# Optimization experiments

Measured on AMD Instinct MI355X. Metric: run time of the kernel, lower is better.

## Reference

```python
import jax, jax.numpy as jnp
import numpy as np

DIM = 256
HEADS = 8
K_RATIO = 0.25


def setup_inputs() -> dict:
    key = jax.random.key(0)
    ks = jax.random.split(key, 5)
    B, C, S = 4, DIM, 2048
    x = jax.random.normal(ks[0], (B, C, S), dtype=jnp.float32)
    # Conv1d(dim, 3*dim, 1, bias=False) weight -> (3*dim, dim)
    W_qkv = jax.random.normal(ks[1], (3 * DIM, DIM), dtype=jnp.float32) * (1.0 / np.sqrt(DIM))
    # depthwise Conv1d(3*dim, 3*dim, 3, groups=3*dim) weight -> (3*dim, 1, 3)
    W_dw = jax.random.normal(ks[2], (3 * DIM, 1, 3), dtype=jnp.float32) * (1.0 / np.sqrt(3))
    # Conv1d(dim, dim, 1, bias=False) weight -> (dim, dim)
    W_proj = jax.random.normal(ks[3], (DIM, DIM), dtype=jnp.float32) * (1.0 / np.sqrt(DIM))
    temperature = jnp.ones((HEADS, 1, 1), dtype=jnp.float32)
    return {"x": x, "W_qkv": W_qkv, "W_dw": W_dw, "W_proj": W_proj,
            "temperature": temperature}


def _l2norm(t, eps=1e-12):
    # F.normalize: x / max(||x||_2, eps)
    n = jnp.sqrt(jnp.sum(t * t, axis=-1, keepdims=True))
    return t / jnp.maximum(n, eps)


def reference(x, W_qkv, W_dw, W_proj, temperature):
    B, C, S = x.shape
    H = temperature.shape[0]
    hd = C // H
    # 1x1 conv == channel matmul
    qkv = jnp.einsum('oc,bcs->bos', W_qkv, x)  # [B, 3C, S]
    # depthwise conv, kernel 3, pad 1
    qkv = jax.lax.conv_general_dilated(
        qkv, W_dw, window_strides=(1,), padding=[(1, 1)],
        dimension_numbers=('NCH', 'OIH', 'NCH'),
        feature_group_count=3 * C)
    q, k, v = jnp.split(qkv, 3, axis=1)  # each [B, C, S]

    def to_heads(t):
        return t.reshape(B, H, hd, S).transpose(0, 1, 3, 2)  # [B, H, S, hd]

    q = _l2norm(to_heads(q))
    k = _l2norm(to_heads(k))
    v = to_heads(v)

    scores = jnp.einsum('bhsc,bhtc->bhst', q, k) * temperature  # [B,H,S,S]

    topk = max(1, min(S, int(np.ceil(K_RATIO * S))))
    vals, idx = jax.lax.top_k(scores, topk)  # [B,H,S,topk]

    # scatter top-k values into a -inf tensor along the last axis
    N = B * H * S
    sparse = jnp.full((N, S), -jnp.inf, dtype=scores.dtype)
    rows = jnp.arange(N)[:, None]
    sparse = sparse.at[rows, idx.reshape(N, topk)].set(vals.reshape(N, topk))
    sparse = jnp.clip(sparse.reshape(B, H, S, S), -10000.0, 10000.0)

    attn = jax.nn.softmax(sparse, axis=-1)  # dropout p=0.0 -> identity
    out = jnp.einsum('bhst,bhtc->bhsc', attn, v)  # [B,H,S,hd]
    out = out.transpose(0, 1, 3, 2).reshape(B, C, S)  # b (head c) s
    return jnp.einsum('oc,bcs->bos', W_proj, out)
```

## Files before the change

### kernel.cpp

```cpp
#include <hip/hip_runtime.h>
#include <math.h>

typedef __attribute__((ext_vector_type(8))) short short8;
typedef __attribute__((ext_vector_type(4))) float f32x4;
typedef __attribute__((ext_vector_type(2))) float f32x2;
typedef __attribute__((ext_vector_type(2))) unsigned int uint2v;
typedef __attribute__((ext_vector_type(4))) unsigned int uint4v;

#define DEV __device__ __forceinline__

static constexpr int B_ = 4, C_ = 256, S_ = 2048, H_ = 8, O3_ = 768;
static constexpr int TOPK = 512;
static constexpr int QT = 16;
static constexpr int QCOLS = 512;
static constexpr int QSTR = 516;
static constexpr int QBUF = 16 * QSTR;
static constexpr int PSTH = 1024;
static constexpr int P1OFF = 2 * QBUF;
static constexpr size_t K3_LDS_BYTES = (size_t)2 * QBUF * 4;
static constexpr int XSTR = 40;

DEV unsigned cvt_pk_bf16(float a, float b) {
  unsigned r;
  asm("v_cvt_pk_bf16_f32 %0, %1, %2" : "=v"(r) : "v"(a), "v"(b));
  return r;
}
DEV unsigned short f2bf1(float f) { return (unsigned short)(cvt_pk_bf16(f, f) & 0xFFFFu); }
DEV float bf2f(unsigned short h) { return __uint_as_float(((unsigned)h) << 16); }
DEV void hilo(float f, unsigned short& h, unsigned short& l) {
  unsigned p = cvt_pk_bf16(f, f);
  h = (unsigned short)p;
  float r = f - __uint_as_float(p << 16);
  l = (unsigned short)(cvt_pk_bf16(r, r) & 0xFFFFu);
}

__global__ void k_convw(const float* __restrict__ wqkv, const float* __restrict__ wproj,
                        unsigned short* __restrict__ wq_hi, unsigned short* __restrict__ wq_lo,
                        unsigned short* __restrict__ wproj_bf) {
  int i = blockIdx.x * 256 + threadIdx.x;
  if (i < O3_ * C_) {
    unsigned short h, l;
    hilo(wqkv[i], h, l);
    wq_hi[i] = h;
    wq_lo[i] = l;
  }
  if (i < C_ * C_) wproj_bf[i] = f2bf1(wproj[i]);
}

__global__ __launch_bounds__(256) void k_qkv(const unsigned short* __restrict__ w_hi,
                                             const unsigned short* __restrict__ w_lo,
                                             const float* __restrict__ x,
                                             float* __restrict__ raw) {
  __shared__ unsigned short xh[2][64 * XSTR];
  __shared__ unsigned short xl[2][64 * XSTR];
  int b = blockIdx.z;
  int m0 = blockIdx.y * 64, n0 = blockIdx.x * 64;
  int tid = threadIdx.x, lane = tid & 63, wid = tid >> 6;
  int l15 = lane & 15, lh = lane >> 4;
  int wm = (wid >> 1) * 32, wn = (wid & 1) * 32;
  int sl = tid & 63, cg = tid >> 6;
  const float* xb = x + (size_t)b * C_ * S_ + n0 + sl;

  f32x4 acc[2][2] = {};
  int mA = m0 + wm + l15;

  auto stage = [&](int k0, int bufi) {
    float f[8];
#pragma unroll
    for (int j = 0; j < 8; ++j)
      f[j] = xb[(size_t)(k0 + cg * 8 + j) * S_];
    unsigned h[4], l[4];
#pragma unroll
    for (int j = 0; j < 4; ++j) {
      h[j] = cvt_pk_bf16(f[2 * j], f[2 * j + 1]);
      float r0 = f[2 * j] - __uint_as_float(h[j] << 16);
      float r1 = f[2 * j + 1] - __uint_as_float(h[j] & 0xFFFF0000u);
      l[j] = cvt_pk_bf16(r0, r1);
    }
    int o = sl * XSTR + cg * 8;
    *(uint4v*)&xh[bufi][o] = uint4v{h[0], h[1], h[2], h[3]};
    *(uint4v*)&xl[bufi][o] = uint4v{l[0], l[1], l[2], l[3]};
  };

  stage(0, 0);
  for (int ks = 0; ks < 8; ++ks) {
    __syncthreads();
    if (ks < 7) stage((ks + 1) * 32, (ks ^ 1) & 1);
    int kk = lh * 8;
    int k0 = ks * 32;
    const unsigned short* bh0 = &xh[ks & 1][(wn + l15) * XSTR + kk];
    const unsigned short* bh1 = &xh[ks & 1][(wn + 16 + l15) * XSTR + kk];
    const unsigned short* bl0 = &xl[ks & 1][(wn + l15) * XSTR + kk];
    const unsigned short* bl1 = &xl[ks & 1][(wn + 16 + l15) * XSTR + kk];
    short8 b0h = *(const short8*)bh0;
    short8 b1h = *(const short8*)bh1;
    short8 b0l = *(const short8*)bl0;
    short8 b1l = *(const short8*)bl1;
    short8 a0h = *(const short8*)(w_hi + (size_t)mA * C_ + k0 + kk);
    short8 a1h = *(const short8*)(w_hi + (size_t)(mA + 16) * C_ + k0 + kk);
    short8 a0l = *(const short8*)(w_lo + (size_t)mA * C_ + k0 + kk);
    short8 a1l = *(const short8*)(w_lo + (size_t)(mA + 16) * C_ + k0 + kk);
    acc[0][0] = __builtin_amdgcn_mfma_f32_16x16x32_bf16(a0h, b0h, acc[0][0], 0, 0, 0);
    acc[0][1] = __builtin_amdgcn_mfma_f32_16x16x32_bf16(a0h, b1h, acc[0][1], 0, 0, 0);
    acc[1][0] = __builtin_amdgcn_mfma_f32_16x16x32_bf16(a1h, b0h, acc[1][0], 0, 0, 0);
    acc[1][1] = __builtin_amdgcn_mfma_f32_16x16x32_bf16(a1h, b1h, acc[1][1], 0, 0, 0);
    acc[0][0] = __builtin_amdgcn_mfma_f32_16x16x32_bf16(a0h, b0l, acc[0][0], 0, 0, 0);
    acc[0][1] = __builtin_amdgcn_mfma_f32_16x16x32_bf16(a0h, b1l, acc[0][1], 0, 0, 0);
    acc[1][0] = __builtin_amdgcn_mfma_f32_16x16x32_bf16(a1h, b0l, acc[1][0], 0, 0, 0);
    acc[1][1] = __builtin_amdgcn_mfma_f32_16x16x32_bf16(a1h, b1l, acc[1][1], 0, 0, 0);
    acc[0][0] = __builtin_amdgcn_mfma_f32_16x16x32_bf16(a0l, b0h, acc[0][0], 0, 0, 0);
    acc[0][1] = __builtin_amdgcn_mfma_f32_16x16x32_bf16(a0l, b1h, acc[0][1], 0, 0, 0);
    acc[1][0] = __builtin_amdgcn_mfma_f32_16x16x32_bf16(a1l, b0h, acc[1][0], 0, 0, 0);
    acc[1][1] = __builtin_amdgcn_mfma_f32_16x16x32_bf16(a1l, b1h, acc[1][1], 0, 0, 0);
  }
  float* rawb = raw + (size_t)b * O3_ * S_;
#pragma unroll
  for (int i = 0; i < 2; ++i)
#pragma unroll
    for (int j = 0; j < 2; ++j)
#pragma unroll
      for (int r = 0; r < 4; ++r) {
        int row = m0 + wm + i * 16 + lh * 4 + r;
        int col = n0 + wn + j * 16 + l15;
        rawb[(size_t)row * S_ + col] = acc[i][j][r];
      }
}

DEV float conv3(const float* __restrict__ rp, const float* __restrict__ w, int s) {
  float a = (s > 0) ? rp[s - 1] : 0.f;
  float b = rp[s];
  float c = (s < S_ - 1) ? rp[s + 1] : 0.f;
  return w[0] * a + w[1] * b + w[2] * c;
}

__global__ __launch_bounds__(256) void k_dwnorm(const float* __restrict__ raw,
                                                const float* __restrict__ wdw,
                                                const float* __restrict__ temp,
                                                unsigned short* __restrict__ q_hi,
                                                unsigned short* __restrict__ q_lo,
                                                unsigned short* __restrict__ k_hi,
                                                unsigned short* __restrict__ k_lo,
                                                unsigned short* __restrict__ vt) {
  int b = blockIdx.z, h = blockIdx.y;
  int tid = threadIdx.x;
  int wave = tid >> 6, lane = tid & 63;
  int dg = lane & 7;
  int sl = lane >> 3;
  int s = blockIdx.x * 32 + wave * 8 + sl;
  const float* rawb = raw + (size_t)b * O3_ * S_;
  float tph = temp[h];
  size_t bh = (size_t)(b * H_ + h);
  float qv[4], kv[4], vv[4];
  float sq = 0.f, sk = 0.f;
#pragma unroll
  for (int dd = 0; dd < 4; ++dd) {
    int d = dg * 4 + dd;
    int oq = h * 32 + d;
    float q = conv3(rawb + (size_t)oq * S_, wdw + oq * 3, s);
    qv[dd] = q; sq += q * q;
    int ok = oq + 256;
    float k = conv3(rawb + (size_t)ok * S_, wdw + ok * 3, s);
    kv[dd] = k; sk += k * k;
    int ov = oq + 512;
    vv[dd] = conv3(rawb + (size_t)ov * S_, wdw + ov * 3, s);
  }
#pragma unroll
  for (int m = 1; m < 8; m <<= 1) {
    sq += __shfl_xor(sq, m);
    sk += __shfl_xor(sk, m);
  }
  float iq = tph / fmaxf(sqrtf(sq), 1e-12f);
  float ik = 1.f / fmaxf(sqrtf(sk), 1e-12f);
  size_t base = (bh * S_ + s) * 32 + dg * 4;

  float q0 = qv[0] * iq, q1 = qv[1] * iq, q2 = qv[2] * iq, q3 = qv[3] * iq;
  unsigned qh01 = cvt_pk_bf16(q0, q1), qh23 = cvt_pk_bf16(q2, q3);
  *(uint2v*)(q_hi + base) = uint2v{qh01, qh23};
  float ql0 = q0 - __uint_as_float(qh01 << 16);
  float ql1 = q1 - __uint_as_float(qh01 & 0xFFFF0000u);
  float ql2 = q2 - __uint_as_float(qh23 << 16);
  float ql3 = q3 - __uint_as_float(qh23 & 0xFFFF0000u);
  *(uint2v*)(q_lo + base) = uint2v{cvt_pk_bf16(ql0, ql1), cvt_pk_bf16(ql2, ql3)};

  float k0 = kv[0] * ik, k1 = kv[1] * ik, k2 = kv[2] * ik, k3 = kv[3] * ik;
  unsigned kh01 = cvt_pk_bf16(k0, k1), kh23 = cvt_pk_bf16(k2, k3);
  *(uint2v*)(k_hi + base) = uint2v{kh01, kh23};
  float kl0 = k0 - __uint_as_float(kh01 << 16);
  float kl1 = k1 - __uint_as_float(kh01 & 0xFFFF0000u);
  float kl2 = k2 - __uint_as_float(kh23 << 16);
  float kl3 = k3 - __uint_as_float(kh23 & 0xFFFF0000u);
  *(uint2v*)(k_lo + base) = uint2v{cvt_pk_bf16(kl0, kl1), cvt_pk_bf16(kl2, kl3)};

#pragma unroll
  for (int dd = 0; dd < 4; ++dd) {
    int d = dg * 4 + dd;
    vt[(bh * 32 + d) * S_ + s] = f2bf1(vv[dd]);
  }
}

__global__ __launch_bounds__(1024, 8) void k_attn(const unsigned short* __restrict__ q_hi,
                                                  const unsigned short* __restrict__ q_lo,
                                                  const unsigned short* __restrict__ k_hi,
                                                  const unsigned short* __restrict__ k_lo,
                                                  const unsigned short* __restrict__ vt,
                                                  unsigned short* __restrict__ ao) {
  extern __shared__ float smem[];
  __shared__ float is_arr[QT];
  unsigned short* Pb = (unsigned short*)smem;
  float* red = smem;
  int bid = blockIdx.x;
  int tile = bid & 127;
  int bh = bid >> 7;
  int q0 = tile * QT;
  int tid = threadIdx.x, lane = tid & 63, wv = tid >> 6;
  int l15 = lane & 15, lh = lane >> 4;
  const unsigned short* vb = vt + (size_t)bh * 32 * S_;

  size_t qoff = ((size_t)bh * S_ + q0 + l15) * 32 + lh * 8;
  short8 ah = *(const short8*)(q_hi + qoff);
  short8 al = *(const short8*)(q_lo + qoff);
  size_t kbase = (size_t)bh * S_ * 32;

  float v[32];

  short8 kh0, kl0, kh1, kl1;
  {
    const unsigned short* kp = k_hi + kbase + (size_t)(wv * 32 + l15) * 32 + lh * 8;
    const unsigned short* lp = k_lo + kbase + (size_t)(wv * 32 + l15) * 32 + lh * 8;
    kh0 = *(const short8*)(kp);       kl0 = *(const short8*)(lp);
    kh1 = *(const short8*)(kp + 512); kl1 = *(const short8*)(lp + 512);
  }
#pragma unroll
  for (int qq = 0; qq < 4; ++qq) {
    float* buf = smem + (qq & 1) * QBUF;
    {
      f32x4 d0 = {}, d1 = {};
      __builtin_amdgcn_s_setprio(1);
      d0 = __builtin_amdgcn_mfma_f32_16x16x32_bf16(ah, kh0, d0, 0, 0, 0);
      d0 = __builtin_amdgcn_mfma_f32_16x16x32_bf16(ah, kl0, d0, 0, 0, 0);
      d0 = __builtin_amdgcn_mfma_f32_16x16x32_bf16(al, kh0, d0, 0, 0, 0);
      d1 = __builtin_amdgcn_mfma_f32_16x16x32_bf16(ah, kh1, d1, 0, 0, 0);
      d1 = __builtin_amdgcn_mfma_f32_16x16x32_bf16(ah, kl1, d1, 0, 0, 0);
      d1 = __builtin_amdgcn_mfma_f32_16x16x32_bf16(al, kh1, d1, 0, 0, 0);
      __builtin_amdgcn_s_setprio(0);
      int tloc = wv * 32 + l15;
#pragma unroll
      for (int r = 0; r < 4; ++r) {
        buf[(lh * 4 + r) * QSTR + tloc] = d0[r];
        buf[(lh * 4 + r) * QSTR + tloc + 16] = d1[r];
      }
      if (qq < 3) {
        int colg = (qq + 1) * QCOLS + wv * 32;
        const unsigned short* kp = k_hi + kbase + (size_t)(colg + l15) * 32 + lh * 8;
        const unsigned short* lp = k_lo + kbase + (size_t)(colg + l15) * 32 + lh * 8;
        kh0 = *(const short8*)(kp);       kl0 = *(const short8*)(lp);
        kh1 = *(const short8*)(kp + 512); kl1 = *(const short8*)(lp + 512);
      }
    }
    __syncthreads();
#pragma unroll
    for (int kk2 = 0; kk2 < 4; ++kk2) {
      f32x2 pr = *(const f32x2*)&buf[wv * QSTR + kk2 * 128 + 2 * lane];
      v[qq * 8 + kk2 * 2] = pr[0];
      v[qq * 8 + kk2 * 2 + 1] = pr[1];
    }
  }

  {
    float vmax = v[0], vmin = v[0], sum = 0.f, sqs = 0.f;
#pragma unroll
    for (int j = 0; j < 32; ++j) {
      vmax = fmaxf(vmax, v[j]); vmin = fminf(vmin, v[j]);
      sum += v[j]; sqs = fmaf(v[j], v[j], sqs);
    }
#pragma unroll
    for (int m = 1; m < 64; m <<= 1) {
      vmax = fmaxf(vmax, __shfl_xor(vmax, m));
      vmin = fminf(vmin, __shfl_xor(vmin, m));
      sum += __shfl_xor(sum, m);
      sqs += __shfl_xor(sqs, m);
    }
    float mu = sum * (1.f / 2048.f);
    float sig = sqrtf(fmaxf(sqs * (1.f / 2048.f) - mu * mu, 0.f));

    float vlo = vmin - 1e-3f, vhi = vmax;
    float flo = 1536.f, fhi = -512.f;
    int chi = 0;
    float T = vhi;
    bool exact = false;
    int lastside = 0;
    float piv = mu + 0.67449f * sig;
    if (!(piv > vlo && piv < vhi)) piv = 0.5f * (vlo + vhi);
    for (int it = 0; it < 32; ++it) {
      int c = 0;
#pragma unroll
      for (int j = 0; j < 32; ++j)
        c += (int)__popcll(__ballot(v[j] > piv));
      if (c == TOPK) { T = piv; exact = true; break; }
      if (c > TOPK) {
        if (lastside == 1) fhi *= 0.5f;
        vlo = piv; flo = (float)(c - TOPK); lastside = 1;
      } else {
        if (lastside == -1) flo *= 0.5f;
        vhi = piv; fhi = (float)(c - TOPK); chi = c; lastside = -1;
      }
      float npiv;
      if (it == 0 && sig > 1e-20f) {
        float z = (piv - mu) / sig;
        float dens = 0.398942f * __expf(-0.5f * z * z) * (2048.f / sig);
        npiv = piv + (float)(c - TOPK) / fmaxf(dens, 1e-6f);
      } else {
        npiv = vhi - fhi * (vhi - vlo) / (fhi - flo);
      }
      if (!(npiv > vlo && npiv < vhi)) npiv = 0.5f * (vlo + vhi);
      if (!(npiv > vlo && npiv < vhi)) break;
      piv = npiv;
    }
    int cntGT = exact ? TOPK : chi;
    if (!exact) T = vhi;

    unsigned selbits = 0;
#pragma unroll
    for (int j = 0; j < 32; ++j)
      if (v[j] > T) selbits |= (1u << j);
    int need = TOPK - cntGT;
    if (need > 0) {
      int base = 0;
      unsigned long long lmask = (lane == 0) ? 0ull : (~0ull >> (64 - lane));
#pragma unroll
      for (int k = 0; k < 16; ++k) {
        bool t0 = (v[2 * k] == T), t1 = (v[2 * k + 1] == T);
        unsigned long long m0 = __ballot(t0);
        unsigned long long m1 = __ballot(t1);
        int before = base + (int)__popcll(m0 & lmask) + (int)__popcll(m1 & lmask);
        int r0 = before;
        int r1 = before + (t0 ? 1 : 0);
        if (t0 && r0 < need) selbits |= (1u << (2 * k));
        if (t1 && r1 < need) selbits |= (1u << (2 * k + 1));
        base += (int)__popcll(m0) + (int)__popcll(m1);
      }
    }

    float ssum = 0.f;
#pragma unroll
    for (int j = 0; j < 32; ++j) {
      float e = ((selbits >> j) & 1u) ? __expf(v[j] - vmax) : 0.f;
      v[j] = e;
      ssum += e;
    }
#pragma unroll
    for (int m = 1; m < 64; m <<= 1) ssum += __shfl_xor(ssum, m);
    if (lane == 0) is_arr[wv] = 1.f / ssum;
  }

  f32x4 acc0 = {}, acc1 = {};
  int swz_w = (wv & 7) << 3;
  int swz_r = (l15 & 7) << 3;
#pragma unroll
  for (int kk = 0; kk < 8; ++kk) {
    int lc = (kk >> 2) * 512 + (kk & 3) * 128 + 2 * lane;
    unsigned pk = cvt_pk_bf16(v[2 * kk], v[2 * kk + 1]);
    *(unsigned*)&Pb[(wv * PSTH + lc) ^ swz_w] = pk;
  }
  __syncthreads();
  {
#pragma unroll
    for (int kk = 0; kk < 8; ++kk) {
      int lc = (kk >> 2) * 512 + (kk & 3) * 128 + 2 * lane;
      unsigned pk = cvt_pk_bf16(v[16 + 2 * kk], v[16 + 2 * kk + 1]);
      *(unsigned*)&Pb[P1OFF + ((wv * PSTH + lc) ^ swz_w)] = pk;
    }
    const unsigned short* v0p = vb + (size_t)l15 * S_ + wv * 64 + lh * 8;
    const unsigned short* v1p = v0p + 16 * S_;
#pragma unroll
    for (int kt = 0; kt < 2; ++kt) {
      int lc = wv * 64 + kt * 32 + lh * 8;
      short8 a = *(const short8*)(Pb + ((l15 * PSTH + lc) ^ swz_r));
      short8 b0 = *(const short8*)(v0p + kt * 32);
      short8 b1 = *(const short8*)(v1p + kt * 32);
      __builtin_amdgcn_s_setprio(1);
      acc0 = __builtin_amdgcn_mfma_f32_16x16x32_bf16(a, b0, acc0, 0, 0, 0);
      acc1 = __builtin_amdgcn_mfma_f32_16x16x32_bf16(a, b1, acc1, 0, 0, 0);
      __builtin_amdgcn_s_setprio(0);
    }
  }
  __syncthreads();
  {
    const unsigned short* v0p = vb + (size_t)l15 * S_ + 1024 + wv * 64 + lh * 8;
    const unsigned short* v1p = v0p + 16 * S_;
#pragma unroll
    for (int kt = 0; kt < 2; ++kt) {
      int lc = wv * 64 + kt * 32 + lh * 8;
      short8 a = *(const short8*)(Pb + P1OFF + ((l15 * PSTH + lc) ^ swz_r));
      short8 b0 = *(const short8*)(v0p + kt * 32);
      short8 b1 = *(const short8*)(v1p + kt * 32);
      __builtin_amdgcn_s_setprio(1);
      acc0 = __builtin_amdgcn_mfma_f32_16x16x32_bf16(a, b0, acc0, 0, 0, 0);
      acc1 = __builtin_amdgcn_mfma_f32_16x16x32_bf16(a, b1, acc1, 0, 0, 0);
      __builtin_amdgcn_s_setprio(0);
    }
  }
  __syncthreads();

#pragma unroll
  for (int r = 0; r < 4; ++r) {
    red[wv * 529 + (lh * 4 + r) * 33 + l15] = acc0[r];
    red[wv * 529 + (lh * 4 + r) * 33 + 16 + l15] = acc1[r];
  }
  __syncthreads();
  if (tid < 512) {
    int row = tid >> 5, d = tid & 31;
    float s = 0.f;
#pragma unroll
    for (int w = 0; w < 16; ++w) s += red[w * 529 + row * 33 + d];
    s *= is_arr[row];
    ao[((size_t)bh * S_ + q0 + row) * 32 + d] = f2bf1(s);
  }
}

__global__ __launch_bounds__(256) void k_proj(const unsigned short* __restrict__ wbf,
                                              const unsigned short* __restrict__ ao,
                                              float* __restrict__ out) {
  int b = blockIdx.z;
  int m0 = blockIdx.y * 64, n0 = blockIdx.x * 64;
  int tid = threadIdx.x, lane = tid & 63, wid = tid >> 6;
  int l15 = lane & 15, lh = lane >> 4;
  int wm = (wid >> 1) * 32, wn = (wid & 1) * 32;
  const unsigned short* aob = ao + (size_t)b * H_ * S_ * 32;
  f32x4 acc[2][2] = {};
  int mA = m0 + wm + l15;
  int nB = n0 + wn + l15;
  for (int k0 = 0; k0 < C_; k0 += 32) {
    int kk = k0 + lh * 8;
    int hh = kk >> 5;
    int dd = kk & 31;
    short8 a0 = *(const short8*)(wbf + (size_t)mA * C_ + kk);
    short8 a1 = *(const short8*)(wbf + (size_t)(mA + 16) * C_ + kk);
    short8 b0 = *(const short8*)(aob + ((size_t)hh * S_ + nB) * 32 + dd);
    short8 b1 = *(const short8*)(aob + ((size_t)hh * S_ + nB + 16) * 32 + dd);
    acc[0][0] = __builtin_amdgcn_mfma_f32_16x16x32_bf16(a0, b0, acc[0][0], 0, 0, 0);
    acc[0][1] = __builtin_amdgcn_mfma_f32_16x16x32_bf16(a0, b1, acc[0][1], 0, 0, 0);
    acc[1][0] = __builtin_amdgcn_mfma_f32_16x16x32_bf16(a1, b0, acc[1][0], 0, 0, 0);
    acc[1][1] = __builtin_amdgcn_mfma_f32_16x16x32_bf16(a1, b1, acc[1][1], 0, 0, 0);
  }
  float* ob = out + (size_t)b * C_ * S_;
#pragma unroll
  for (int i = 0; i < 2; ++i)
#pragma unroll
    for (int j = 0; j < 2; ++j)
#pragma unroll
      for (int r = 0; r < 4; ++r) {
        int row = m0 + wm + i * 16 + lh * 4 + r;
        int col = n0 + wn + j * 16 + l15;
        ob[(size_t)row * S_ + col] = acc[i][j][r];
      }
}

extern "C" void kernel_launch(void* const* d_in, const int* in_sizes, int n_in,
                              void* d_out, int out_size, void* d_ws, size_t ws_size,
                              hipStream_t stream) {
  const float* x = (const float*)d_in[0];
  const float* wqkv = (const float*)d_in[1];
  const float* wdw = (const float*)d_in[2];
  const float* wproj = (const float*)d_in[3];
  const float* temp = (const float*)d_in[4];
  float* out = (float*)d_out;

  char* ws = (char*)d_ws;
  size_t off = 0;
  auto alloc = [&](size_t bytes) -> void* {
    void* p = ws + off;
    off += (bytes + 255) & ~(size_t)255;
    return p;
  };
  unsigned short* wq_hi    = (unsigned short*)alloc((size_t)O3_ * C_ * 2);
  unsigned short* wq_lo    = (unsigned short*)alloc((size_t)O3_ * C_ * 2);
  unsigned short* wproj_bf = (unsigned short*)alloc((size_t)C_ * C_ * 2);
  float*          raw      = (float*)alloc((size_t)B_ * O3_ * S_ * 4);
  unsigned short* q_hi     = (unsigned short*)alloc((size_t)B_ * H_ * S_ * 32 * 2);
  unsigned short* q_lo     = (unsigned short*)alloc((size_t)B_ * H_ * S_ * 32 * 2);
  unsigned short* k_hi     = (unsigned short*)alloc((size_t)B_ * H_ * S_ * 32 * 2);
  unsigned short* k_lo     = (unsigned short*)alloc((size_t)B_ * H_ * S_ * 32 * 2);
  unsigned short* vt       = (unsigned short*)alloc((size_t)B_ * H_ * 32 * S_ * 2);
  unsigned short* ao       = (unsigned short*)raw;

  (void)hipFuncSetAttribute(reinterpret_cast<const void*>(k_attn),
                            hipFuncAttributeMaxDynamicSharedMemorySize, (int)K3_LDS_BYTES);

  k_convw<<<dim3((O3_ * C_ + 255) / 256), dim3(256), 0, stream>>>(wqkv, wproj, wq_hi, wq_lo, wproj_bf);
  k_qkv<<<dim3(S_ / 64, O3_ / 64, B_), dim3(256), 0, stream>>>(wq_hi, wq_lo, x, raw);
  k_dwnorm<<<dim3(S_ / 32, H_, B_), dim3(256), 0, stream>>>(raw, wdw, temp, q_hi, q_lo, k_hi, k_lo, vt);
  k_attn<<<dim3(B_ * H_ * (S_ / QT)), dim3(1024), K3_LDS_BYTES, stream>>>(q_hi, q_lo, k_hi, k_lo, vt, ao);
  k_proj<<<dim3(S_ / 64, C_ / 64, B_), dim3(256), 0, stream>>>(wproj_bf, ao, out);
}
```

Before: 252.0 us.

## Fuse QKV projection with depthwise conv and L2 normalization in one kernel

Merges the QKV 1x1-conv GEMM and the depthwise conv plus normalization kernels into one kernel per (batch, head, 64-column tile). The block computes its head's q/k/v rows, including a one-column halo, into shared memory and then applies the conv and normalization directly. This removes the large fp32 intermediate buffer round-trip through global memory and one launch. In exchange it recomputes halo columns, re-reads x once per head, and uses a less vectorized staging loop.

Result: no change. 247.2 us (-1.9%).

```diff
diff --git a/kernel.cpp b/kernel.cpp
--- a/kernel.cpp
+++ b/kernel.cpp
@@ -5,7 +5,6 @@
 typedef __attribute__((ext_vector_type(4))) float f32x4;
 typedef __attribute__((ext_vector_type(2))) float f32x2;
 typedef __attribute__((ext_vector_type(2))) unsigned int uint2v;
-typedef __attribute__((ext_vector_type(4))) unsigned int uint4v;
 
 #define DEV __device__ __forceinline__
 
@@ -18,7 +17,10 @@
 static constexpr int PSTH = 1024;
 static constexpr int P1OFF = 2 * QBUF;
 static constexpr size_t K3_LDS_BYTES = (size_t)2 * QBUF * 4;
-static constexpr int XSTR = 40;
+
+static constexpr int XQSTR = 40;
+static constexpr int NROWS = 80;
+static constexpr int RSTR = 85;
 
 DEV unsigned cvt_pk_bf16(float a, float b) {
   unsigned r;
@@ -26,7 +28,6 @@
   return r;
 }
 DEV unsigned short f2bf1(float f) { return (unsigned short)(cvt_pk_bf16(f, f) & 0xFFFFu); }
-DEV float bf2f(unsigned short h) { return __uint_as_float(((unsigned)h) << 16); }
 DEV void hilo(float f, unsigned short& h, unsigned short& l) {
   unsigned p = cvt_pk_bf16(f, f);
   h = (unsigned short)p;
@@ -47,154 +48,131 @@
   if (i < C_ * C_) wproj_bf[i] = f2bf1(wproj[i]);
 }
 
-__global__ __launch_bounds__(256) void k_qkv(const unsigned short* __restrict__ w_hi,
-                                             const unsigned short* __restrict__ w_lo,
-                                             const float* __restrict__ x,
-                                             float* __restrict__ raw) {
-  __shared__ unsigned short xh[2][64 * XSTR];
-  __shared__ unsigned short xl[2][64 * XSTR];
+__global__ __launch_bounds__(512) void k_qkvf(const unsigned short* __restrict__ w_hi,
+                                              const unsigned short* __restrict__ w_lo,
+                                              const float* __restrict__ x,
+                                              const float* __restrict__ wdw,
+                                              const float* __restrict__ temp,
+                                              unsigned short* __restrict__ q_hi,
+                                              unsigned short* __restrict__ q_lo,
+                                              unsigned short* __restrict__ k_hi,
+                                              unsigned short* __restrict__ k_lo,
+                                              unsigned short* __restrict__ vt) {
+  __shared__ unsigned short xh[2][NROWS * XQSTR];
+  __shared__ unsigned short xl[2][NROWS * XQSTR];
+  __shared__ float raw[96 * RSTR];
+  int n0 = blockIdx.x * 64;
+  int h = blockIdx.y;
   int b = blockIdx.z;
-  int m0 = blockIdx.y * 64, n0 = blockIdx.x * 64;
-  int tid = threadIdx.x, lane = tid & 63, wid = tid >> 6;
+  int tid = threadIdx.x, lane = tid & 63, wv = tid >> 6;
   int l15 = lane & 15, lh = lane >> 4;
-  int wm = (wid >> 1) * 32, wn = (wid & 1) * 32;
-  int sl = tid & 63, cg = tid >> 6;
-  const float* xb = x + (size_t)b * C_ * S_ + n0 + sl;
-
-  f32x4 acc[2][2] = {};
-  int mA = m0 + wm + l15;
-
-  auto stage = [&](int k0, int bufi) {
-    float f[8];
-#pragma unroll
-    for (int j = 0; j < 8; ++j)
-      f[j] = xb[(size_t)(k0 + cg * 8 + j) * S_];
-    unsigned h[4], l[4];
-#pragma unroll
-    for (int j = 0; j < 4; ++j) {
-      h[j] = cvt_pk_bf16(f[2 * j], f[2 * j + 1]);
-      float r0 = f[2 * j] - __uint_as_float(h[j] << 16);
-      float r1 = f[2 * j + 1] - __uint_as_float(h[j] & 0xFFFF0000u);
-      l[j] = cvt_pk_bf16(r0, r1);
-    }
-    int o = sl * XSTR + cg * 8;
-    *(uint4v*)&xh[bufi][o] = uint4v{h[0], h[1], h[2], h[3]};
-    *(uint4v*)&xl[bufi][o] = uint4v{l[0], l[1], l[2], l[3]};
+  const float* xb = x + (size_t)b * C_ * S_;
+
+  auto stage = [&](int ks, int bufi) {
+    int k0 = ks * 32;
+    for (int i = tid; i < 66 * 32; i += 512) {
+      int kk = i / 66;
+      int sr = i - kk * 66;
+      int s = n0 - 1 + sr;
+      float f = (s >= 0 && s < S_) ? xb[(size_t)(k0 + kk) * S_ + s] : 0.f;
+      unsigned short hh, ll;
+      hilo(f, hh, ll);
+      xh[bufi][sr * XQSTR + kk] = hh;
+      xl[bufi][sr * XQSTR + kk] = ll;
+    }
   };
+
+  int mt = wv;
+  int obase = (mt >> 1) * 256 + h * 32 + (mt & 1) * 16;
+  f32x4 acc[5] = {};
 
   stage(0, 0);
   for (int ks = 0; ks < 8; ++ks) {
     __syncthreads();
-    if (ks < 7) stage((ks + 1) * 32, (ks ^ 1) & 1);
-    int kk = lh * 8;
-    int k0 = ks * 32;
-    const unsigned short* bh0 = &xh[ks & 1][(wn + l15) * XSTR + kk];
-    const unsigned short* bh1 = &xh[ks & 1][(wn + 16 + l15) * XSTR + kk];
-    const unsigned short* bl0 = &xl[ks & 1][(wn + l15) * XSTR + kk];
-    const unsigned short* bl1 = &xl[ks & 1][(wn + 16 + l15) * XSTR + kk];
-    short8 b0h = *(const short8*)bh0;
-    short8 b1h = *(const short8*)bh1;
-    short8 b0l = *(const short8*)bl0;
-    short8 b1l = *(const short8*)bl1;
-    short8 a0h = *(const short8*)(w_hi + (size_t)mA * C_ + k0 + kk);
-    short8 a1h = *(const short8*)(w_hi + (size_t)(mA + 16) * C_ + k0 + kk);
-    short8 a0l = *(const short8*)(w_lo + (size_t)mA * C_ + k0 + kk);
-    short8 a1l = *(const short8*)(w_lo + (size_t)(mA + 16) * C_ + k0 + kk);
-    acc[0][0] = __builtin_amdgcn_mfma_f32_16x16x32_bf16(a0h, b0h, acc[0][0], 0, 0, 0);
-    acc[0][1] = __builtin_amdgcn_mfma_f32_16x16x32_bf16(a0h, b1h, acc[0][1], 0, 0, 0);
-    acc[1][0] = __builtin_amdgcn_mfma_f32_16x16x32_bf16(a1h, b0h, acc[1][0], 0, 0, 0);
-    acc[1][1] = __builtin_amdgcn_mfma_f32_16x16x32_bf16(a1h, b1h, acc[1][1], 0, 0, 0);
-    acc[0][0] = __builtin_amdgcn_mfma_f32_16x16x32_bf16(a0h, b0l, acc[0][0], 0, 0, 0);
-    acc[0][1] = __builtin_amdgcn_mfma_f32_16x16x32_bf16(a0h, b1l, acc[0][1], 0, 0, 0);
-    acc[1][0] = __builtin_amdgcn_mfma_f32_16x16x32_bf16(a1h, b0l, acc[1][0], 0, 0, 0);
-    acc[1][1] = __builtin_amdgcn_mfma_f32_16x16x32_bf16(a1h, b1l, acc[1][1], 0, 0, 0);
-    acc[0][0] = __builtin_amdgcn_mfma_f32_16x16x32_bf16(a0l, b0h, acc[0][0], 0, 0, 0);
-    acc[0][1] = __builtin_amdgcn_mfma_f32_16x16x32_bf16(a0l, b1h, acc[0][1], 0, 0, 0);
-    acc[1][0] = __builtin_amdgcn_mfma_f32_16x16x32_bf16(a1l, b0h, acc[1][0], 0, 0, 0);
-    acc[1][1] = __builtin_amdgcn_mfma_f32_16x16x32_bf16(a1l, b1h, acc[1][1], 0, 0, 0);
-  }
-  float* rawb = raw + (size_t)b * O3_ * S_;
-#pragma unroll
-  for (int i = 0; i < 2; ++i)
-#pragma unroll
-    for (int j = 0; j < 2; ++j)
-#pragma unroll
-      for (int r = 0; r < 4; ++r) {
-        int row = m0 + wm + i * 16 + lh * 4 + r;
-        int col = n0 + wn + j * 16 + l15;
-        rawb[(size_t)row * S_ + col] = acc[i][j][r];
-      }
-}
-
-DEV float conv3(const float* __restrict__ rp, const float* __restrict__ w, int s) {
-  float a = (s > 0) ? rp[s - 1] : 0.f;
-  float b = rp[s];
-  float c = (s < S_ - 1) ? rp[s + 1] : 0.f;
-  return w[0] * a + w[1] * b + w[2] * c;
-}
-
-__global__ __launch_bounds__(256) void k_dwnorm(const float* __restrict__ raw,
-                                                const float* __restrict__ wdw,
-                                                const float* __restrict__ temp,
-                                                unsigned short* __restrict__ q_hi,
-                                                unsigned short* __restrict__ q_lo,
-                                                unsigned short* __restrict__ k_hi,
-                                                unsigned short* __restrict__ k_lo,
-                                                unsigned short* __restrict__ vt) {
-  int b = blockIdx.z, h = blockIdx.y;
-  int tid = threadIdx.x;
-  int wave = tid >> 6, lane = tid & 63;
-  int dg = lane & 7;
-  int sl = lane >> 3;
-  int s = blockIdx.x * 32 + wave * 8 + sl;
-  const float* rawb = raw + (size_t)b * O3_ * S_;
-  float tph = temp[h];
-  size_t bh = (size_t)(b * H_ + h);
-  float qv[4], kv[4], vv[4];
-  float sq = 0.f, sk = 0.f;
-#pragma unroll
-  for (int dd = 0; dd < 4; ++dd) {
-    int d = dg * 4 + dd;
-    int oq = h * 32 + d;
-    float q = conv3(rawb + (size_t)oq * S_, wdw + oq * 3, s);
-    qv[dd] = q; sq += q * q;
-    int ok = oq + 256;
-    float k = conv3(rawb + (size_t)ok * S_, wdw + ok * 3, s);
-    kv[dd] = k; sk += k * k;
-    int ov = oq + 512;
-    vv[dd] = conv3(rawb + (size_t)ov * S_, wdw + ov * 3, s);
-  }
-#pragma unroll
-  for (int m = 1; m < 8; m <<= 1) {
-    sq += __shfl_xor(sq, m);
-    sk += __shfl_xor(sk, m);
-  }
-  float iq = tph / fmaxf(sqrtf(sq), 1e-12f);
-  float ik = 1.f / fmaxf(sqrtf(sk), 1e-12f);
-  size_t base = (bh * S_ + s) * 32 + dg * 4;
-
-  float q0 = qv[0] * iq, q1 = qv[1] * iq, q2 = qv[2] * iq, q3 = qv[3] * iq;
-  unsigned qh01 = cvt_pk_bf16(q0, q1), qh23 = cvt_pk_bf16(q2, q3);
-  *(uint2v*)(q_hi + base) = uint2v{qh01, qh23};
-  float ql0 = q0 - __uint_as_float(qh01 << 16);
-  float ql1 = q1 - __uint_as_float(qh01 & 0xFFFF0000u);
-  float ql2 = q2 - __uint_as_float(qh23 << 16);
-  float ql3 = q3 - __uint_as_float(qh23 & 0xFFFF0000u);
-  *(uint2v*)(q_lo + base) = uint2v{cvt_pk_bf16(ql0, ql1), cvt_pk_bf16(ql2, ql3)};
-
-  float k0 = kv[0] * ik, k1 = kv[1] * ik, k2 = kv[2] * ik, k3 = kv[3] * ik;
-  unsigned kh01 = cvt_pk_bf16(k0, k1), kh23 = cvt_pk_bf16(k2, k3);
-  *(uint2v*)(k_hi + base) = uint2v{kh01, kh23};
-  float kl0 = k0 - __uint_as_float(kh01 << 16);
-  float kl1 = k1 - __uint_as_float(kh01 & 0xFFFF0000u);
-  float kl2 = k2 - __uint_as_float(kh23 << 16);
-  float kl3 = k3 - __uint_as_float(kh23 & 0xFFFF0000u);
-  *(uint2v*)(k_lo + base) = uint2v{cvt_pk_bf16(kl0, kl1), cvt_pk_bf16(kl2, kl3)};
-
-#pragma unroll
-  for (int dd = 0; dd < 4; ++dd) {
-    int d = dg * 4 + dd;
-    vt[(bh * 32 + d) * S_ + s] = f2bf1(vv[dd]);
+    if (ks < 7) stage(ks + 1, (ks + 1) & 1);
+    if (wv < 6) {
+      int kk = lh * 8;
+      short8 ahf = *(const short8*)(w_hi + (size_t)(obase + l15) * C_ + ks * 32 + kk);
+      short8 alf = *(const short8*)(w_lo + (size_t)(obase + l15) * C_ + ks * 32 + kk);
+#pragma unroll
+      for (int n = 0; n < 5; ++n) {
+        const unsigned short* bh_ = &xh[ks & 1][(n * 16 + l15) * XQSTR + kk];
+        const unsigned short* bl_ = &xl[ks & 1][(n * 16 + l15) * XQSTR + kk];
+        short8 bh = *(const short8*)bh_;
+        short8 bl = *(const short8*)bl_;
+        acc[n] = __builtin_amdgcn_mfma_f32_16x16x32_bf16(ahf, bh, acc[n], 0, 0, 0);
+        acc[n] = __builtin_amdgcn_mfma_f32_16x16x32_bf16(ahf, bl, acc[n], 0, 0, 0);
+        acc[n] = __builtin_amdgcn_mfma_f32_16x16x32_bf16(alf, bh, acc[n], 0, 0, 0);
+      }
+    }
+  }
+  __syncthreads();
+  if (wv < 6) {
+#pragma unroll
+    for (int n = 0; n < 5; ++n)
+#pragma unroll
+      for (int r = 0; r < 4; ++r)
+        raw[(mt * 16 + lh * 4 + r) * RSTR + n * 16 + l15] = acc[n][r];
+  }
+  __syncthreads();
+
+  {
+    int s_loc = tid >> 3;
+    int dg = tid & 7;
+    int s = n0 + s_loc;
+    float tph = temp[h];
+    size_t bh_ = (size_t)(b * H_ + h);
+    float qv[4], kv[4], vv[4];
+    float sq = 0.f, sk = 0.f;
+#pragma unroll
+    for (int dd = 0; dd < 4; ++dd) {
+      int d = dg * 4 + dd;
+      int oq = h * 32 + d;
+      const float* wq = wdw + oq * 3;
+      const float* wk = wdw + (oq + 256) * 3;
+      const float* wvv = wdw + (oq + 512) * 3;
+      const float* rq = &raw[d * RSTR + s_loc];
+      const float* rk = &raw[(32 + d) * RSTR + s_loc];
+      const float* rv = &raw[(64 + d) * RSTR + s_loc];
+      float q = wq[0] * rq[0] + wq[1] * rq[1] + wq[2] * rq[2];
+      float k = wk[0] * rk[0] + wk[1] * rk[1] + wk[2] * rk[2];
+      float v = wvv[0] * rv[0] + wvv[1] * rv[1] + wvv[2] * rv[2];
+      qv[dd] = q; sq += q * q;
+      kv[dd] = k; sk += k * k;
+      vv[dd] = v;
+    }
+#pragma unroll
+    for (int m = 1; m < 8; m <<= 1) {
+      sq += __shfl_xor(sq, m);
+      sk += __shfl_xor(sk, m);
+    }
+    float iq = tph / fmaxf(sqrtf(sq), 1e-12f);
+    float ik = 1.f / fmaxf(sqrtf(sk), 1e-12f);
+    size_t base = (bh_ * S_ + s) * 32 + dg * 4;
+
+    float q0 = qv[0] * iq, q1 = qv[1] * iq, q2 = qv[2] * iq, q3 = qv[3] * iq;
+    unsigned qh01 = cvt_pk_bf16(q0, q1), qh23 = cvt_pk_bf16(q2, q3);
+    *(uint2v*)(q_hi + base) = uint2v{qh01, qh23};
+    float ql0 = q0 - __uint_as_float(qh01 << 16);
+    float ql1 = q1 - __uint_as_float(qh01 & 0xFFFF0000u);
+    float ql2 = q2 - __uint_as_float(qh23 << 16);
+    float ql3 = q3 - __uint_as_float(qh23 & 0xFFFF0000u);
+    *(uint2v*)(q_lo + base) = uint2v{cvt_pk_bf16(ql0, ql1), cvt_pk_bf16(ql2, ql3)};
+
+    float k0 = kv[0] * ik, k1 = kv[1] * ik, k2 = kv[2] * ik, k3 = kv[3] * ik;
+    unsigned kh01 = cvt_pk_bf16(k0, k1), kh23 = cvt_pk_bf16(k2, k3);
+    *(uint2v*)(k_hi + base) = uint2v{kh01, kh23};
+    float kl0 = k0 - __uint_as_float(kh01 << 16);
+    float kl1 = k1 - __uint_as_float(kh01 & 0xFFFF0000u);
+    float kl2 = k2 - __uint_as_float(kh23 << 16);
+    float kl3 = k3 - __uint_as_float(kh23 & 0xFFFF0000u);
+    *(uint2v*)(k_lo + base) = uint2v{cvt_pk_bf16(kl0, kl1), cvt_pk_bf16(kl2, kl3)};
+
+#pragma unroll
+    for (int dd = 0; dd < 4; ++dd) {
+      int d = dg * 4 + dd;
+      vt[(bh_ * 32 + d) * S_ + s] = f2bf1(vv[dd]);
+    }
   }
 }
 
@@ -476,20 +454,19 @@
   unsigned short* wq_hi    = (unsigned short*)alloc((size_t)O3_ * C_ * 2);
   unsigned short* wq_lo    = (unsigned short*)alloc((size_t)O3_ * C_ * 2);
   unsigned short* wproj_bf = (unsigned short*)alloc((size_t)C_ * C_ * 2);
-  float*          raw      = (float*)alloc((size_t)B_ * O3_ * S_ * 4);
   unsigned short* q_hi     = (unsigned short*)alloc((size_t)B_ * H_ * S_ * 32 * 2);
   unsigned short* q_lo     = (unsigned short*)alloc((size_t)B_ * H_ * S_ * 32 * 2);
   unsigned short* k_hi     = (unsigned short*)alloc((size_t)B_ * H_ * S_ * 32 * 2);
   unsigned short* k_lo     = (unsigned short*)alloc((size_t)B_ * H_ * S_ * 32 * 2);
   unsigned short* vt       = (unsigned short*)alloc((size_t)B_ * H_ * 32 * S_ * 2);
-  unsigned short* ao       = (unsigned short*)raw;
+  unsigned short* ao       = (unsigned short*)alloc((size_t)B_ * H_ * S_ * 32 * 2);
 
   (void)hipFuncSetAttribute(reinterpret_cast<const void*>(k_attn),
                             hipFuncAttributeMaxDynamicSharedMemorySize, (int)K3_LDS_BYTES);
 
   k_convw<<<dim3((O3_ * C_ + 255) / 256), dim3(256), 0, stream>>>(wqkv, wproj, wq_hi, wq_lo, wproj_bf);
-  k_qkv<<<dim3(S_ / 64, O3_ / 64, B_), dim3(256), 0, stream>>>(wq_hi, wq_lo, x, raw);
-  k_dwnorm<<<dim3(S_ / 32, H_, B_), dim3(256), 0, stream>>>(raw, wdw, temp, q_hi, q_lo, k_hi, k_lo, vt);
+  k_qkvf<<<dim3(S_ / 64, H_, B_), dim3(512), 0, stream>>>(wq_hi, wq_lo, x, wdw, temp,
+                                                          q_hi, q_lo, k_hi, k_lo, vt);
   k_attn<<<dim3(B_ * H_ * (S_ / QT)), dim3(1024), K3_LDS_BYTES, stream>>>(q_hi, q_lo, k_hi, k_lo, vt, ao);
   k_proj<<<dim3(S_ / 64, C_ / 64, B_), dim3(256), 0, stream>>>(wproj_bf, ao, out);
 }
```
